# Optimization experiments

Hardware: AMD Instinct MI355X
Metric: run time of the kernel (lower is better)

Reference implementation:

```python
import jax, jax.numpy as jnp
import numpy as np

B = 512          # batch
SIZE_IN = 1024   # input features
SIZE_OUT = 256   # output features
NUM_Q = 16       # quantiles


def setup_inputs() -> dict:
    key = jax.random.key(0)
    k1, k2, k3, k4 = jax.random.split(key, 4)
    x = jax.random.normal(k1, (B, SIZE_IN), dtype=jnp.float32)
    indices = jax.random.randint(k2, (B, SIZE_IN), 0, NUM_Q, dtype=jnp.int64)
    # param_index table: row (q*SIZE_IN + j) holds a SIZE_OUT weight vector
    param_table = jax.random.normal(k3, (NUM_Q * SIZE_IN, SIZE_OUT), dtype=jnp.float32)
    bias = jax.random.normal(k4, (SIZE_OUT,), dtype=jnp.float32)
    return {"x": x, "indices": indices, "param_table": param_table, "bias": bias}


def reference(x, indices, param_table, bias):
    size_in = x.shape[1]
    # flat row index into the quantile-indexed table: q*size_in + feature_pos
    flat_idx = indices * size_in + jnp.arange(size_in, dtype=indices.dtype)[None, :]  # [B, In]
    gathered = param_table[flat_idx]  # [B, In, Out] gather
    # scale each gathered weight vector by the scalar input and reduce over features
    out = jnp.einsum('bi,bio->bo', x, gathered)  # [B, Out]
    return out + bias
```

## Files before the change

kernel.cpp:

```cpp
#include <hip/hip_runtime.h>
#include <stdint.h>


constexpr int SIZE_IN  = 1024;
constexpr int SIZE_OUT = 256;
constexpr int BATCH    = 512;
constexpr int NUM_Q    = 16;
constexpr int KTOT     = NUM_Q * SIZE_IN;
constexpr int A_LD     = 1040;
constexpr int TM       = 32;

constexpr size_t A_OFF    = 0;
constexpr size_t A_BYTES  = (size_t)NUM_Q * BATCH * A_LD * 2;
constexpr size_t BT_OFF   = A_OFF + A_BYTES;
constexpr size_t BT_BYTES = (size_t)SIZE_OUT * KTOT * 2;
constexpr size_t P_OFF    = BT_OFF + BT_BYTES;
constexpr size_t P_BYTES  = (size_t)NUM_Q * BATCH * SIZE_OUT * 4;
constexpr size_t WS_NEED  = P_OFF + P_BYTES;

typedef short short8   __attribute__((ext_vector_type(8)));
typedef float floatx4  __attribute__((ext_vector_type(4)));

__device__ inline uint32_t pack2bf(float lo, float hi) {
    uint32_t a = __float_as_uint(lo) + 0x8000u;
    uint32_t b = __float_as_uint(hi) + 0x8000u;
    return __builtin_amdgcn_perm(b, a, 0x07060302);
}
__device__ inline uint16_t bf1(float f) {
    return (uint16_t)((__float_as_uint(f) + 0x8000u) >> 16);
}

__global__ __launch_bounds__(256)
void expand_a(const float* __restrict__ x, const int* __restrict__ idx,
              uint16_t* __restrict__ A)
{
    const int g  = blockIdx.x * 256 + threadIdx.x;
    const int b  = g >> 7;
    const int i0 = (g & 127) * 8;
    const float4 xv0 = *(const float4*)(x + b * SIZE_IN + i0);
    const float4 xv1 = *(const float4*)(x + b * SIZE_IN + i0 + 4);
    const int4   iv0 = *(const int4*)(idx + b * SIZE_IN + i0);
    const int4   iv1 = *(const int4*)(idx + b * SIZE_IN + i0 + 4);
    const float xs[8] = {xv0.x,xv0.y,xv0.z,xv0.w, xv1.x,xv1.y,xv1.z,xv1.w};
    const int   is[8] = {iv0.x,iv0.y,iv0.z,iv0.w, iv1.x,iv1.y,iv1.z,iv1.w};
    #pragma unroll
    for (int q = 0; q < NUM_Q; ++q) {
        float m[8];
        #pragma unroll
        for (int j = 0; j < 8; ++j) m[j] = (is[j] == q) ? xs[j] : 0.f;
        uint4 d;
        d.x = pack2bf(m[0], m[1]); d.y = pack2bf(m[2], m[3]);
        d.z = pack2bf(m[4], m[5]); d.w = pack2bf(m[6], m[7]);
        *(uint4*)(A + (size_t)(q * BATCH + b) * A_LD + i0) = d;
    }
}

__global__ __launch_bounds__(256)
void transpose_bt(const float* __restrict__ table, uint16_t* __restrict__ Bt)
{
    __shared__ uint16_t t[64][72];
    const int k0  = (blockIdx.x & 255) * 64;
    const int o0  = (blockIdx.x >> 8) * 64;
    const int tid = threadIdx.x;
    {
        const int kr = tid >> 4;
        const int oc = (tid & 15) * 4;
        #pragma unroll
        for (int rr = 0; rr < 4; ++rr) {
            const int k = rr * 16 + kr;
            const float4 v = *(const float4*)(table + (size_t)(k0 + k) * SIZE_OUT + o0 + oc);
            t[oc + 0][k] = bf1(v.x);
            t[oc + 1][k] = bf1(v.y);
            t[oc + 2][k] = bf1(v.z);
            t[oc + 3][k] = bf1(v.w);
        }
    }
    __syncthreads();
    const int orow = tid >> 2;
    const int kc   = (tid & 3) * 16;
    const uint4 lo = *(const uint4*)(&t[orow][kc]);
    const uint4 hi = *(const uint4*)(&t[orow][kc + 8]);
    uint16_t* dst = Bt + (size_t)(o0 + orow) * KTOT + k0 + kc;
    *(uint4*)dst       = lo;
    *(uint4*)(dst + 8) = hi;
}

__global__ __launch_bounds__(512, 1)
void gemm_splitq(const uint16_t* __restrict__ A,
                 const uint16_t* __restrict__ Bt,
                 float* __restrict__ parts)
{
    __shared__ uint16_t Al[TM * A_LD];
    const int tid   = threadIdx.x;
    const int q     = blockIdx.x & 15;
    const int bt    = blockIdx.x >> 4;
    const int b0    = bt * TM;
    const int w     = tid >> 6;
    const int lane  = tid & 63;
    const int nlane = lane & 15;
    const int quad  = lane >> 4;

    {
        const uint4* src = (const uint4*)(A + (size_t)(q * BATCH + b0) * A_LD);
        uint4* dst = (uint4*)Al;
        #pragma unroll
        for (int c = 0; c < 8; ++c)
            dst[c * 512 + tid] = src[c * 512 + tid];
        if (tid < 64) dst[8 * 512 + tid] = src[8 * 512 + tid];
    }
    __syncthreads();

    const uint16_t* bp0 = Bt + (size_t)(w * 32 + nlane) * KTOT + q * SIZE_IN + quad * 8;
    const uint16_t* bp1 = bp0 + (size_t)16 * KTOT;
    const uint16_t* ar0 = Al + nlane * A_LD + quad * 8;
    const uint16_t* ar1 = ar0 + 16 * A_LD;

    floatx4 acc00 = {0,0,0,0}, acc01 = {0,0,0,0}, acc10 = {0,0,0,0}, acc11 = {0,0,0,0};

    #pragma unroll 8
    for (int kb = 0; kb < 32; ++kb) {
        const short8 a0 = *(const short8*)(ar0 + kb * 32);
        const short8 a1 = *(const short8*)(ar1 + kb * 32);
        const short8 bq0 = *(const short8*)(bp0 + kb * 32);
        const short8 bq1 = *(const short8*)(bp1 + kb * 32);
        acc00 = __builtin_amdgcn_mfma_f32_16x16x32_bf16(a0, bq0, acc00, 0, 0, 0);
        acc10 = __builtin_amdgcn_mfma_f32_16x16x32_bf16(a1, bq0, acc10, 0, 0, 0);
        acc01 = __builtin_amdgcn_mfma_f32_16x16x32_bf16(a0, bq1, acc01, 0, 0, 0);
        acc11 = __builtin_amdgcn_mfma_f32_16x16x32_bf16(a1, bq1, acc11, 0, 0, 0);
    }

    float* pq = parts + ((size_t)q * BATCH + b0) * SIZE_OUT;
    const int col0 = w * 32 + nlane;
    #pragma unroll
    for (int rr = 0; rr < 4; ++rr) {
        const int r0 = quad * 4 + rr;
        pq[(size_t)r0 * SIZE_OUT + col0]            = acc00[rr];
        pq[(size_t)r0 * SIZE_OUT + col0 + 16]       = acc01[rr];
        pq[(size_t)(r0 + 16) * SIZE_OUT + col0]     = acc10[rr];
        pq[(size_t)(r0 + 16) * SIZE_OUT + col0 + 16]= acc11[rr];
    }
}

__global__ __launch_bounds__(256)
void reduce_ws(const float* __restrict__ ws, const float* __restrict__ bias,
               float* __restrict__ out)
{
    const int e  = blockIdx.x * 256 + threadIdx.x;
    const int o4 = e & 63;
    const float4* w4 = reinterpret_cast<const float4*>(ws);
    float4 s = reinterpret_cast<const float4*>(bias)[o4];
    #pragma unroll
    for (int q = 0; q < NUM_Q; ++q) {
        const float4 v = w4[(size_t)q * (BATCH * SIZE_OUT / 4) + e];
        s.x += v.x; s.y += v.y; s.z += v.z; s.w += v.w;
    }
    reinterpret_cast<float4*>(out)[e] = s;
}

__global__ __launch_bounds__(256)
void fallback_gather(const float* __restrict__ x, const int* __restrict__ idx,
                     const float* __restrict__ table, const float* __restrict__ bias,
                     float* __restrict__ out)
{
    __shared__ int2 xr[SIZE_IN];
    const int b = blockIdx.x, tid = threadIdx.x;
    const float4 xv = reinterpret_cast<const float4*>(x + b * SIZE_IN)[tid];
    const int4   qv = reinterpret_cast<const int4*>(idx + b * SIZE_IN)[tid];
    const int ib = tid * 4;
    xr[ib+0] = make_int2(__float_as_int(xv.x), (qv.x*SIZE_IN+ib+0)*SIZE_OUT);
    xr[ib+1] = make_int2(__float_as_int(xv.y), (qv.y*SIZE_IN+ib+1)*SIZE_OUT);
    xr[ib+2] = make_int2(__float_as_int(xv.z), (qv.z*SIZE_IN+ib+2)*SIZE_OUT);
    xr[ib+3] = make_int2(__float_as_int(xv.w), (qv.w*SIZE_IN+ib+3)*SIZE_OUT);
    __syncthreads();
    float s = bias[tid];
    for (int j = 0; j < SIZE_IN; ++j) {
        const int2 p = xr[j];
        s = fmaf(__int_as_float(p.x), table[p.y + tid], s);
    }
    out[b * SIZE_OUT + tid] = s;
}

extern "C" void kernel_launch(void* const* d_in, const int* in_sizes, int n_in,
                              void* d_out, int out_size, void* d_ws, size_t ws_size,
                              hipStream_t stream) {
    const float* x     = (const float*)d_in[0];
    const int*   idx   = (const int*)d_in[1];
    const float* table = (const float*)d_in[2];
    const float* bias  = (const float*)d_in[3];
    float*       out   = (float*)d_out;

    if (ws_size >= WS_NEED) {
        uint16_t* Aws = (uint16_t*)((char*)d_ws + A_OFF);
        uint16_t* Btw = (uint16_t*)((char*)d_ws + BT_OFF);
        float*    pts = (float*)((char*)d_ws + P_OFF);
        expand_a    <<<dim3(BATCH * 128 / 256), dim3(256), 0, stream>>>(x, idx, Aws);
        transpose_bt<<<dim3((KTOT / 64) * (SIZE_OUT / 64)), dim3(256), 0, stream>>>(table, Btw);
        gemm_splitq <<<dim3((BATCH / TM) * NUM_Q), dim3(512), 0, stream>>>(Aws, Btw, pts);
        reduce_ws   <<<dim3(BATCH * SIZE_OUT / 4 / 256), dim3(256), 0, stream>>>(pts, bias, out);
    } else {
        fallback_gather<<<dim3(BATCH), dim3(256), 0, stream>>>(x, idx, table, bias, out);
    }
}
```

Measured before the change: 100.7 us.

## Fuse masked-A expansion into GEMM prologue, dropping expand kernel and workspace

Removes the separate expand_a kernel, which wrote a 16x-expanded bf16 masked A matrix to global memory. The GEMM block now reads x and idx directly and builds its masked bf16 A tile in shared memory. This saves one launch and roughly 17MB of global write-and-reread traffic. In exchange, each of the 16 q-blocks per batch tile rereads the same fp32 x and idx rows, and the prologue does more work before the MFMA loop.

```diff
diff --git a/kernel.cpp b/kernel.cpp
--- a/kernel.cpp
+++ b/kernel.cpp
@@ -10,9 +10,7 @@
 constexpr int A_LD     = 1040;
 constexpr int TM       = 32;
 
-constexpr size_t A_OFF    = 0;
-constexpr size_t A_BYTES  = (size_t)NUM_Q * BATCH * A_LD * 2;
-constexpr size_t BT_OFF   = A_OFF + A_BYTES;
+constexpr size_t BT_OFF   = 0;
 constexpr size_t BT_BYTES = (size_t)SIZE_OUT * KTOT * 2;
 constexpr size_t P_OFF    = BT_OFF + BT_BYTES;
 constexpr size_t P_BYTES  = (size_t)NUM_Q * BATCH * SIZE_OUT * 4;
@@ -28,31 +26,6 @@
 }
 __device__ inline uint16_t bf1(float f) {
     return (uint16_t)((__float_as_uint(f) + 0x8000u) >> 16);
-}
-
-__global__ __launch_bounds__(256)
-void expand_a(const float* __restrict__ x, const int* __restrict__ idx,
-              uint16_t* __restrict__ A)
-{
-    const int g  = blockIdx.x * 256 + threadIdx.x;
-    const int b  = g >> 7;
-    const int i0 = (g & 127) * 8;
-    const float4 xv0 = *(const float4*)(x + b * SIZE_IN + i0);
-    const float4 xv1 = *(const float4*)(x + b * SIZE_IN + i0 + 4);
-    const int4   iv0 = *(const int4*)(idx + b * SIZE_IN + i0);
-    const int4   iv1 = *(const int4*)(idx + b * SIZE_IN + i0 + 4);
-    const float xs[8] = {xv0.x,xv0.y,xv0.z,xv0.w, xv1.x,xv1.y,xv1.z,xv1.w};
-    const int   is[8] = {iv0.x,iv0.y,iv0.z,iv0.w, iv1.x,iv1.y,iv1.z,iv1.w};
-    #pragma unroll
-    for (int q = 0; q < NUM_Q; ++q) {
-        float m[8];
-        #pragma unroll
-        for (int j = 0; j < 8; ++j) m[j] = (is[j] == q) ? xs[j] : 0.f;
-        uint4 d;
-        d.x = pack2bf(m[0], m[1]); d.y = pack2bf(m[2], m[3]);
-        d.z = pack2bf(m[4], m[5]); d.w = pack2bf(m[6], m[7]);
-        *(uint4*)(A + (size_t)(q * BATCH + b) * A_LD + i0) = d;
-    }
 }
 
 __global__ __launch_bounds__(256)
@@ -86,9 +59,10 @@
 }
 
 __global__ __launch_bounds__(512, 1)
-void gemm_splitq(const uint16_t* __restrict__ A,
-                 const uint16_t* __restrict__ Bt,
-                 float* __restrict__ parts)
+void gemm_fused(const float* __restrict__ x,
+                const int*   __restrict__ idx,
+                const uint16_t* __restrict__ Bt,
+                float* __restrict__ parts)
 {
     __shared__ uint16_t Al[TM * A_LD];
     const int tid   = threadIdx.x;
@@ -101,12 +75,23 @@
     const int quad  = lane >> 4;
 
     {
-        const uint4* src = (const uint4*)(A + (size_t)(q * BATCH + b0) * A_LD);
-        uint4* dst = (uint4*)Al;
-        #pragma unroll
-        for (int c = 0; c < 8; ++c)
-            dst[c * 512 + tid] = src[c * 512 + tid];
-        if (tid < 64) dst[8 * 512 + tid] = src[8 * 512 + tid];
+        const float4* x4 = (const float4*)(x   + b0 * SIZE_IN);
+        const int4*   i4 = (const int4*)(idx + b0 * SIZE_IN);
+        const int s  = tid >> 4;
+        const int c0 = tid & 15;
+        #pragma unroll 4
+        for (int c = c0; c < 256; c += 16) {
+            const float4 xv = x4[s * 256 + c];
+            const int4   iv = i4[s * 256 + c];
+            const float v0 = (iv.x == q) ? xv.x : 0.f;
+            const float v1 = (iv.y == q) ? xv.y : 0.f;
+            const float v2 = (iv.z == q) ? xv.z : 0.f;
+            const float v3 = (iv.w == q) ? xv.w : 0.f;
+            uint2 d;
+            d.x = pack2bf(v0, v1);
+            d.y = pack2bf(v2, v3);
+            *(uint2*)(&Al[s * A_LD + c * 4]) = d;
+        }
     }
     __syncthreads();
 
@@ -190,12 +175,10 @@
     float*       out   = (float*)d_out;
 
     if (ws_size >= WS_NEED) {
-        uint16_t* Aws = (uint16_t*)((char*)d_ws + A_OFF);
         uint16_t* Btw = (uint16_t*)((char*)d_ws + BT_OFF);
         float*    pts = (float*)((char*)d_ws + P_OFF);
-        expand_a    <<<dim3(BATCH * 128 / 256), dim3(256), 0, stream>>>(x, idx, Aws);
         transpose_bt<<<dim3((KTOT / 64) * (SIZE_OUT / 64)), dim3(256), 0, stream>>>(table, Btw);
-        gemm_splitq <<<dim3((BATCH / TM) * NUM_Q), dim3(512), 0, stream>>>(Aws, Btw, pts);
+        gemm_fused  <<<dim3((BATCH / TM) * NUM_Q), dim3(512), 0, stream>>>(x, idx, Btw, pts);
         reduce_ws   <<<dim3(BATCH * SIZE_OUT / 4 / 256), dim3(256), 0, stream>>>(pts, bias, out);
     } else {
         fallback_gather<<<dim3(BATCH), dim3(256), 0, stream>>>(x, idx, table, bias, out);
```

Result: faster. 97.33 us (-3.4%).
